# Kernel tuning notes

Hardware: AMD Instinct MI355X
Metric: run time of the kernel (lower is better)

The kernel has to match this reference:

```python
import jax, jax.numpy as jnp
import numpy as np
import math

NB = 4           # num_bands
EPS = 1e-5       # LayerNorm eps


def _dwconv(x, w):
    # depthwise Conv1d, padding=1, kernel=3. x: [b, t, c], w: [c, 1, k]
    c = x.shape[-1]
    y = jax.lax.conv_general_dilated(
        x.transpose(0, 2, 1), w, window_strides=(1,), padding=[(1, 1)],
        dimension_numbers=('NCH', 'OIH', 'NCH'), feature_group_count=c)
    return y.transpose(0, 2, 1)


def _ln(x, g, b):
    m = jnp.mean(x, axis=-1, keepdims=True)
    v = jnp.mean(jnp.square(x - m), axis=-1, keepdims=True)
    return (x - m) * jax.lax.rsqrt(v + EPS) * g + b


def _attn(x, mem, qw, qc, kw, kc, vw, vc, ow, pw, prev_qk):
    # x, mem: [b, w, c]
    b, w, c = x.shape
    d = c // NB
    q = _dwconv(x @ qw.T, qc).reshape(b, w, NB, d).transpose(0, 2, 1, 3)      # [b,nb,w,d]
    k = _dwconv(mem @ kw.T, kc).reshape(b, w, NB, d).transpose(0, 2, 3, 1)    # [b,nb,d,w]
    v = _dwconv(mem @ vw.T, vc).reshape(b, w, NB, d).transpose(0, 2, 1, 3)    # [b,nb,w,d]
    # skewed relative-position bias: matmul + pad + transpose + slice
    p = jnp.einsum('bnwd,dt->bnwt', q, pw[:, :w])                              # [b,nb,w,w]
    p = jnp.pad(p, ((0, 0), (0, 0), (0, 0), (1, 0)))                           # pad last dim left
    p = p.transpose(0, 1, 3, 2)[:, :, 1:, :]                                   # skew
    qk = (jnp.einsum('bnwd,bndt->bnwt', q, k) + p) / math.sqrt(c)
    if prev_qk is not None:
        qk = qk + prev_qk
    a = jnp.einsum('bnwt,bntd->bnwd', jax.nn.softmax(qk, axis=-1), v)
    a = a.transpose(0, 2, 1, 3).reshape(b, w, c)
    return a @ ow.T, qk


def setup_inputs() -> dict:
    key = jax.random.key(0)
    ks = jax.random.split(key, 32)
    B, CH, BINS, W, FF = 4, 8, 1024, 1024, 2048
    s = 0.02
    inp = {
        'x': jax.random.normal(ks[0], (B, CH, BINS, W), jnp.float32),
        'mem': jax.random.normal(ks[1], (B, CH, BINS, W), jnp.float32),
        'prev_qk1': jax.random.normal(ks[2], (B, NB, W, W), jnp.float32),
        'prev_qk2': jax.random.normal(ks[3], (B, NB, W, W), jnp.float32),
        'ip_w': jax.random.normal(ks[4], (CH,), jnp.float32) * s,
        'ip_b': jnp.zeros((1,), jnp.float32),
        'mp_w': jax.random.normal(ks[5], (CH,), jnp.float32) * s,
        'mp_b': jnp.zeros((1,), jnp.float32),
        'ln1_g': jnp.ones((BINS,), jnp.float32), 'ln1_b': jnp.zeros((BINS,), jnp.float32),
        'ln2_g': jnp.ones((BINS,), jnp.float32), 'ln2_b': jnp.zeros((BINS,), jnp.float32),
        'ln3_g': jnp.ones((BINS,), jnp.float32), 'ln3_b': jnp.zeros((BINS,), jnp.float32),
        'a1_qw': jax.random.normal(ks[6], (BINS, BINS), jnp.float32) * s,
        'a1_qc': jax.random.normal(ks[7], (BINS, 1, 3), jnp.float32) * 0.3,
        'a1_kw': jax.random.normal(ks[8], (BINS, BINS), jnp.float32) * s,
        'a1_kc': jax.random.normal(ks[9], (BINS, 1, 3), jnp.float32) * 0.3,
        'a1_vw': jax.random.normal(ks[10], (BINS, BINS), jnp.float32) * s,
        'a1_vc': jax.random.normal(ks[11], (BINS, 1, 3), jnp.float32) * 0.3,
        'a1_ow': jax.random.normal(ks[12], (BINS, BINS), jnp.float32) * s,
        'a1_pw': jax.random.normal(ks[13], (BINS // NB, W), jnp.float32),
        'a2_qw': jax.random.normal(ks[14], (BINS, BINS), jnp.float32) * s,
        'a2_qc': jax.random.normal(ks[15], (BINS, 1, 3), jnp.float32) * 0.3,
        'a2_kw': jax.random.normal(ks[16], (BINS, BINS), jnp.float32) * s,
        'a2_kc': jax.random.normal(ks[17], (BINS, 1, 3), jnp.float32) * 0.3,
        'a2_vw': jax.random.normal(ks[18], (BINS, BINS), jnp.float32) * s,
        'a2_vc': jax.random.normal(ks[19], (BINS, 1, 3), jnp.float32) * 0.3,
        'a2_ow': jax.random.normal(ks[20], (BINS, BINS), jnp.float32) * s,
        'a2_pw': jax.random.normal(ks[21], (BINS // NB, W), jnp.float32),
        'l1_w': jax.random.normal(ks[22], (FF, BINS), jnp.float32) * s,
        'l2_w': jax.random.normal(ks[23], (BINS, FF), jnp.float32) * s,
    }
    return inp


def reference(x, mem, prev_qk1, prev_qk2, ip_w, ip_b, mp_w, mp_b,
              ln1_g, ln1_b, ln2_g, ln2_b, ln3_g, ln3_b,
              a1_qw, a1_qc, a1_kw, a1_kc, a1_vw, a1_vc, a1_ow, a1_pw,
              a2_qw, a2_qc, a2_kw, a2_kc, a2_vw, a2_vc, a2_ow, a2_pw,
              l1_w, l2_w):
    # 1x1 Conv2d to 1 channel then [b, w, bins] layout
    xs = jnp.einsum('bchw,c->bwh', x, ip_w) + ip_b    # [b, w, bins]
    ms = jnp.einsum('bchw,c->bwh', mem, mp_w) + mp_b
    # self-attention with prev_qk residual
    h, qk1 = _attn(_ln(xs, ln1_g, ln1_b), _ln(xs, ln1_g, ln1_b),
                   a1_qw, a1_qc, a1_kw, a1_kc, a1_vw, a1_vc, a1_ow, a1_pw, prev_qk1)
    xs = xs + h
    # cross-attention against mem
    h, qk2 = _attn(_ln(xs, ln2_g, ln2_b), ms,
                   a2_qw, a2_qc, a2_kw, a2_kc, a2_vw, a2_vc, a2_ow, a2_pw, prev_qk2)
    xs = xs + h
    # squared-ReLU FFN
    h = _ln(xs, ln3_g, ln3_b)
    h = jnp.square(jax.nn.relu(h @ l1_w.T)) @ l2_w.T
    xs = xs + h
    out = xs.transpose(0, 2, 1)[:, None]              # [b, 1, bins, w]
    return (out, qk1, qk2)
```

## Files before the change

kernel.cpp:

```cpp
#include <hip/hip_runtime.h>
#include <stdint.h>

typedef unsigned short u16;
typedef __bf16 bfv8 __attribute__((ext_vector_type(8)));
typedef float f32x4 __attribute__((ext_vector_type(4)));
typedef unsigned short u16x8 __attribute__((ext_vector_type(8)));

#define DI __device__ __forceinline__

DI u16 f2bf(float f) {
  union { float f; unsigned u; } c; c.f = f;
  unsigned r = c.u + 0x7FFFu + ((c.u >> 16) & 1u);
  return (u16)(r >> 16);
}
DI float bf2f(u16 b) {
  union { unsigned u; float f; } c; c.u = ((unsigned)b) << 16;
  return c.f;
}

enum { EPI_BF16 = 0, EPI_RELU2 = 1, EPI_ADDF32 = 2, EPI_QK = 3 };

#define GLDS(g, l)                                                              \
  __builtin_amdgcn_global_load_lds((const __attribute__((address_space(1))) void*)(g), \
                                   (__attribute__((address_space(3))) void*)(l), 16, 0, 0)

#define VMCNT_BAR(N)                                        \
  do {                                                      \
    asm volatile("s_waitcnt vmcnt(" #N ")" ::: "memory");   \
    __builtin_amdgcn_sched_barrier(0);                      \
    __builtin_amdgcn_s_barrier();                           \
    __builtin_amdgcn_sched_barrier(0);                      \
  } while (0)

template <int EPI, bool KSPLIT, int BN>
__global__ __launch_bounds__(512) void gemm256(
    const u16* __restrict__ Aq, const u16* __restrict__ Akv, int asplit,
    long a1q, long a1r, int lda1,
    const u16* __restrict__ A2, int lda2,
    const u16* __restrict__ B1, long b1q, long b1r, int ldb1,
    const u16* __restrict__ B2, long b2q, long b2r, int ldb2,
    int K, int ksp,
    void* __restrict__ Cv, long cq, long cr, int ldc,
    const float* __restrict__ extra, long eq, int lde,
    float scale)
{
  constexpr int NJ = BN / 64;
  constexpr int NBL = BN / 64;
  constexpr int SS = 8192 + BN * 64;
  constexpr int LPS = 2 + NBL;
  __shared__ __align__(16) u16 lds[3 * SS];
  const int tid = threadIdx.x;
  const int wid = tid >> 6, lane = tid & 63;
  const long zq = blockIdx.z >> 2, zr = blockIdx.z & 3;
  const int m0 = blockIdx.y * 128, n0 = blockIdx.x * BN;
  const u16* Ab = ((n0 >= asplit) ? Akv : Aq) + zq * a1q + zr * a1r;
  const u16* Bb = B1 + zq * b1q + zr * b1r;
  const u16* B2b = KSPLIT ? (B2 + zq * b2q + zr * b2r) : (const u16*)nullptr;
  const int wm = (wid >> 2) * 64, wn = (wid & 3) * (BN / 4);
  const int fr = lane & 15, fq = lane >> 4;

  f32x4 acc[4][NJ];
#pragma unroll
  for (int i = 0; i < 4; ++i)
#pragma unroll
    for (int j = 0; j < NJ; ++j)
      acc[i][j] = (f32x4){0.f, 0.f, 0.f, 0.f};

  const int nt = K >> 6;

  auto STAGE = [&](int tt, int sb) {
    const int k0 = tt << 6;
    u16* Ld = &lds[sb * SS];
    const u16* Asrc; int la; const u16* Bsrc; int lb;
    if (!KSPLIT || k0 < ksp) { Asrc = Ab + k0; la = lda1; Bsrc = Bb + k0; lb = ldb1; }
    else { Asrc = A2 + (k0 - ksp); la = lda2; Bsrc = B2b + (k0 - ksp); lb = ldb2; }
#pragma unroll
    for (int l = 0; l < 2; ++l) {
      int idx = (l << 9) + tid;
      int row = idx >> 3;
      int sc = ((idx & 7) ^ (row & 7)) << 3;
      GLDS(Asrc + (size_t)(m0 + row) * la + sc,
           Ld + (((l << 3) + wid) << 9));
    }
#pragma unroll
    for (int l = 0; l < NBL; ++l) {
      int idx = (l << 9) + tid;
      int row = idx >> 3;
      int sc = ((idx & 7) ^ (row & 7)) << 3;
      GLDS(Bsrc + (size_t)(n0 + row) * lb + sc,
           Ld + 8192 + (((l << 3) + wid) << 9));
    }
  };

  auto COMPUTE = [&](int cb) {
    const u16* As = &lds[cb * SS];
    const u16* Bs = As + 8192;
#pragma unroll
    for (int ks = 0; ks < 2; ++ks) {
      bfv8 av[4];
#pragma unroll
      for (int i = 0; i < 4; ++i) {
        int ra = wm + i * 16 + fr;
        int ca = (((ks << 2) + fq) ^ (ra & 7)) << 3;
        av[i] = *(const bfv8*)&As[(ra << 6) + ca];
      }
#pragma unroll
      for (int nh = 0; nh < NJ / 2; ++nh) {
        bfv8 bv[2];
#pragma unroll
        for (int j = 0; j < 2; ++j) {
          int rb = wn + (nh << 5) + (j << 4) + fr;
          int cb2 = (((ks << 2) + fq) ^ (rb & 7)) << 3;
          bv[j] = *(const bfv8*)&Bs[(rb << 6) + cb2];
        }
        __builtin_amdgcn_s_setprio(1);
#pragma unroll
        for (int i = 0; i < 4; ++i) {
          acc[i][(nh << 1)] = __builtin_amdgcn_mfma_f32_16x16x32_bf16(av[i], bv[0], acc[i][(nh << 1)], 0, 0, 0);
          acc[i][(nh << 1) + 1] = __builtin_amdgcn_mfma_f32_16x16x32_bf16(av[i], bv[1], acc[i][(nh << 1) + 1], 0, 0, 0);
        }
        __builtin_amdgcn_s_setprio(0);
      }
    }
  };

  STAGE(0, 0);
  STAGE(1, 1);
  if constexpr (LPS == 6) VMCNT_BAR(6); else VMCNT_BAR(4);
  int cur = 0;
  for (int t = 0; t < nt; ++t) {
    if (t + 2 < nt) {
      int stg = cur + 2; if (stg >= 3) stg -= 3;
      STAGE(t + 2, stg);
      COMPUTE(cur);
      if constexpr (LPS == 6) VMCNT_BAR(6); else VMCNT_BAR(4);
    } else if (t + 1 < nt) {
      COMPUTE(cur);
      VMCNT_BAR(0);
    } else {
      COMPUTE(cur);
    }
    cur = (cur == 2) ? 0 : cur + 1;
  }

  if constexpr (EPI == EPI_BF16 || EPI == EPI_RELU2) {
    u16* Cb = (u16*)Cv + zq * cq + zr * cr;
#pragma unroll
    for (int i = 0; i < 4; ++i)
#pragma unroll
      for (int j = 0; j < NJ; ++j)
#pragma unroll
        for (int r = 0; r < 4; ++r) {
          int row = m0 + wm + i * 16 + (fq << 2) + r;
          int col = n0 + wn + j * 16 + fr;
          float v = acc[i][j][r];
          if constexpr (EPI == EPI_RELU2) { v = fmaxf(v, 0.f); v = v * v; }
          Cb[(size_t)row * ldc + col] = f2bf(v);
        }
  } else if constexpr (EPI == EPI_ADDF32) {
    float* Cb = (float*)Cv + zq * cq + zr * cr;
#pragma unroll
    for (int i = 0; i < 4; ++i)
#pragma unroll
      for (int j = 0; j < NJ; ++j)
#pragma unroll
        for (int r = 0; r < 4; ++r) {
          int row = m0 + wm + i * 16 + (fq << 2) + r;
          int col = n0 + wn + j * 16 + fr;
          Cb[(size_t)row * ldc + col] += acc[i][j][r];
        }
  } else {
    float* Cb = (float*)Cv + zq * cq + zr * cr;
    const float* Eb = extra + (size_t)blockIdx.z * eq;
#pragma unroll
    for (int i = 0; i < 4; ++i)
#pragma unroll
      for (int j = 0; j < NJ; ++j)
#pragma unroll
        for (int r = 0; r < 4; ++r) {
          int row = m0 + wm + i * 16 + (fq << 2) + r;
          int col = n0 + wn + j * 16 + fr;
          Cb[(size_t)row * ldc + col] = acc[i][j][r] * scale + Eb[(size_t)row * lde + col];
        }
  }
}

__global__ __launch_bounds__(256) void proj2v_kernel(const float* __restrict__ x,
                                                     const float* __restrict__ memp,
                                                     const float* __restrict__ ipw,
                                                     const float* __restrict__ ipb,
                                                     const float* __restrict__ mpw,
                                                     const float* __restrict__ mpb,
                                                     float* __restrict__ xs,
                                                     u16* __restrict__ msb)
{
  __shared__ float lt[64][65];
  int task = blockIdx.z >> 2;
  int b = blockIdx.z & 3;
  const float* src = task ? memp : x;
  const float* w8 = task ? mpw : ipw;
  float bias = task ? mpb[0] : ipb[0];
  int h0 = blockIdx.y * 64, w0 = blockIdx.x * 64;
  int tx = threadIdx.x & 15;
  int hy = threadIdx.x >> 4;
#pragma unroll
  for (int p = 0; p < 4; ++p) {
    int h = h0 + hy + p * 16;
    f32x4 acc = {bias, bias, bias, bias};
#pragma unroll
    for (int c = 0; c < 8; ++c) {
      f32x4 v = *(const f32x4*)&src[(((size_t)b * 8 + c) * 1024 + h) * 1024 + w0 + tx * 4];
      float wc = w8[c];
      acc.x += v.x * wc; acc.y += v.y * wc; acc.z += v.z * wc; acc.w += v.w * wc;
    }
    int hl = hy + p * 16;
    lt[tx * 4 + 0][hl] = acc.x;
    lt[tx * 4 + 1][hl] = acc.y;
    lt[tx * 4 + 2][hl] = acc.z;
    lt[tx * 4 + 3][hl] = acc.w;
  }
  __syncthreads();
  int hx = threadIdx.x & 15;
  int wy = threadIdx.x >> 4;
#pragma unroll
  for (int p = 0; p < 4; ++p) {
    int wl = wy + p * 16;
    f32x4 v;
    v.x = lt[wl][hx * 4 + 0];
    v.y = lt[wl][hx * 4 + 1];
    v.z = lt[wl][hx * 4 + 2];
    v.w = lt[wl][hx * 4 + 3];
    size_t o = ((size_t)b * 1024 + w0 + wl) * 1024 + h0 + hx * 4;
    if (task) {
      ushort4 ov;
      ov.x = f2bf(v.x); ov.y = f2bf(v.y); ov.z = f2bf(v.z); ov.w = f2bf(v.w);
      *(ushort4*)&msb[o] = ov;
    } else {
      *(f32x4*)&xs[o] = v;
    }
  }
}

__global__ __launch_bounds__(256) void ln_kernel(const float* __restrict__ x,
                                                 const float* __restrict__ g,
                                                 const float* __restrict__ b,
                                                 u16* __restrict__ out)
{
  int row = blockIdx.x, tid = threadIdx.x;
  float4 v = ((const float4*)(x + (size_t)row * 1024))[tid];
  float s = v.x + v.y + v.z + v.w;
  float s2 = v.x * v.x + v.y * v.y + v.z * v.z + v.w * v.w;
#pragma unroll
  for (int o = 32; o; o >>= 1) { s += __shfl_down(s, o); s2 += __shfl_down(s2, o); }
  __shared__ float rs[4], rs2[4];
  int wid = tid >> 6, lane = tid & 63;
  if (lane == 0) { rs[wid] = s; rs2[wid] = s2; }
  __syncthreads();
  s = rs[0] + rs[1] + rs[2] + rs[3];
  s2 = rs2[0] + rs2[1] + rs2[2] + rs2[3];
  float mean = s * (1.f / 1024.f);
  float var = s2 * (1.f / 1024.f) - mean * mean;
  float rstd = rsqrtf(var + 1e-5f);
  float4 gv = ((const float4*)g)[tid];
  float4 bv = ((const float4*)b)[tid];
  ushort4 o;
  o.x = f2bf((v.x - mean) * rstd * gv.x + bv.x);
  o.y = f2bf((v.y - mean) * rstd * gv.y + bv.y);
  o.z = f2bf((v.z - mean) * rstd * gv.z + bv.z);
  o.w = f2bf((v.w - mean) * rstd * gv.w + bv.w);
  ((ushort4*)out)[(size_t)row * 256 + tid] = o;
}

__global__ __launch_bounds__(128) void dwconv_qk_kernel(const u16* __restrict__ qkv,
                                                        const float* __restrict__ qc,
                                                        const float* __restrict__ kc,
                                                        u16* __restrict__ Qc,
                                                        u16* __restrict__ Kc)
{
  int sel = blockIdx.y;
  int row = blockIdx.x;
  int t = row & 1023;
  int c0 = threadIdx.x * 8;
  const u16* r0 = qkv + (size_t)row * 3072 + (sel << 10) + c0;
  const float* wc = sel ? kc : qc;
  u16* dst = (sel ? Kc : Qc) + (size_t)row * 1024 + c0;
  u16x8 zv = {0, 0, 0, 0, 0, 0, 0, 0};
  u16x8 xm = zv, xp = zv;
  if (t > 0) xm = *(const u16x8*)(r0 - 3072);
  u16x8 xc = *(const u16x8*)r0;
  if (t < 1023) xp = *(const u16x8*)(r0 + 3072);
  u16x8 o;
#pragma unroll
  for (int j = 0; j < 8; ++j) {
    int c = c0 + j;
    float v = bf2f(xm[j]) * wc[c * 3 + 0] + bf2f(xc[j]) * wc[c * 3 + 1] + bf2f(xp[j]) * wc[c * 3 + 2];
    o[j] = f2bf(v);
  }
  *(u16x8*)dst = o;
}

__global__ __launch_bounds__(1024) void dwconv_t_kernel(const u16* __restrict__ qkv,
                                                        const float* __restrict__ wc,
                                                        u16* __restrict__ out)
{
  __shared__ float tile[32][33];
  int b = blockIdx.z;
  int t = blockIdx.x * 32 + threadIdx.y;
  int c = blockIdx.y * 32 + threadIdx.x;
  size_t base = ((size_t)b * 1024 + t) * 3072 + 2048 + c;
  float xm = (t > 0) ? bf2f(qkv[base - 3072]) : 0.f;
  float xc = bf2f(qkv[base]);
  float xp = (t < 1023) ? bf2f(qkv[base + 3072]) : 0.f;
  tile[threadIdx.y][threadIdx.x] = xm * wc[c * 3 + 0] + xc * wc[c * 3 + 1] + xp * wc[c * 3 + 2];
  __syncthreads();
  int c2 = blockIdx.y * 32 + threadIdx.y;
  int t2 = blockIdx.x * 32 + threadIdx.x;
  int z = b * 4 + (c2 >> 8);
  out[((size_t)z * 256 + (c2 & 255)) * 1024 + t2] = f2bf(tile[threadIdx.x][threadIdx.y]);
}

__global__ __launch_bounds__(256) void softmax_kernel(const float* __restrict__ qk,
                                                      u16* __restrict__ P)
{
  size_t row = blockIdx.x;
  int tid = threadIdx.x;
  float4 v = ((const float4*)(qk + row * 1024))[tid];
  float m = fmaxf(fmaxf(v.x, v.y), fmaxf(v.z, v.w));
#pragma unroll
  for (int o = 32; o; o >>= 1) m = fmaxf(m, __shfl_down(m, o));
  __shared__ float red[4];
  int wid = tid >> 6, lane = tid & 63;
  if (lane == 0) red[wid] = m;
  __syncthreads();
  m = fmaxf(fmaxf(red[0], red[1]), fmaxf(red[2], red[3]));
  float e0 = __expf(v.x - m), e1 = __expf(v.y - m), e2 = __expf(v.z - m), e3 = __expf(v.w - m);
  float s = e0 + e1 + e2 + e3;
#pragma unroll
  for (int o = 32; o; o >>= 1) s += __shfl_down(s, o);
  __syncthreads();
  if (lane == 0) red[wid] = s;
  __syncthreads();
  s = red[0] + red[1] + red[2] + red[3];
  float rinv = 1.f / s;
  ushort4 o;
  o.x = f2bf(e0 * rinv); o.y = f2bf(e1 * rinv); o.z = f2bf(e2 * rinv); o.w = f2bf(e3 * rinv);
  ((ushort4*)P)[row * 256 + tid] = o;
}

struct CastJobs { const float* s[12]; u16* d[12]; };
__global__ __launch_bounds__(256) void cast12_kernel(CastJobs J)
{
  int j = blockIdx.y;
  int i = blockIdx.x * 256 + threadIdx.x;
  float4 v = ((const float4*)J.s[j])[i];
  ushort4 o;
  o.x = f2bf(v.x); o.y = f2bf(v.y); o.z = f2bf(v.z); o.w = f2bf(v.w);
  ((ushort4*)J.d[j])[i] = o;
}

__global__ __launch_bounds__(1024) void pwt_kernel(const float* __restrict__ pw,
                                                   u16* __restrict__ pwT)
{
  __shared__ float tile[32][33];
  int d = blockIdx.y * 32 + threadIdx.y;
  int t = blockIdx.x * 32 + threadIdx.x;
  tile[threadIdx.y][threadIdx.x] = pw[(size_t)d * 1024 + t];
  __syncthreads();
  int t2 = blockIdx.x * 32 + threadIdx.y;
  int d2 = blockIdx.y * 32 + threadIdx.x;
  pwT[(size_t)t2 * 256 + d2] = f2bf(tile[threadIdx.x][threadIdx.y]);
}

__global__ __launch_bounds__(1024) void tout_kernel(const float* __restrict__ xs,
                                                    float* __restrict__ out)
{
  __shared__ float tile[32][33];
  int b = blockIdx.z;
  int w = blockIdx.x * 32 + threadIdx.y;
  int h = blockIdx.y * 32 + threadIdx.x;
  tile[threadIdx.y][threadIdx.x] = xs[((size_t)b * 1024 + w) * 1024 + h];
  __syncthreads();
  int h2 = blockIdx.y * 32 + threadIdx.y;
  int w2 = blockIdx.x * 32 + threadIdx.x;
  out[((size_t)b * 1024 + h2) * 1024 + w2] = tile[threadIdx.x][threadIdx.y];
}

static void run_attn(hipStream_t stream, float* xs, const u16* qsrc, const u16* kvsrc, int asplit,
                     u16* QKVraw, u16* Qc, u16* Kc, u16* Vt, u16* P, u16* Am,
                     const u16* wqkv, const u16* wo, const u16* pwt,
                     const float* qc, const float* kc, const float* vc,
                     const float* prevqk, float* qko)
{
  dim3 blk(512);
  gemm256<EPI_BF16, false, 256><<<dim3(12, 32, 1), blk, 0, stream>>>(
      qsrc, kvsrc, asplit, 0, 0, 1024, nullptr, 0,
      wqkv, 0, 0, 1024, nullptr, 0, 0, 0,
      1024, 0, QKVraw, 0, 0, 3072, nullptr, 0, 0, 1.f);
  dwconv_qk_kernel<<<dim3(4096, 2), 128, 0, stream>>>(QKVraw, qc, kc, Qc, Kc);
  dwconv_t_kernel<<<dim3(32, 32, 4), dim3(32, 32), 0, stream>>>(QKVraw, vc, Vt);
  gemm256<EPI_QK, true, 256><<<dim3(4, 8, 16), blk, 0, stream>>>(
      Qc, Qc, 1 << 30, 1048576, 256, 1024, pwt, 256,
      Kc, 1048576, 256, 1024, Qc, 1048576, 256, 1024,
      512, 256, qko, 4194304, 1048576, 1024, prevqk, 1048576, 1024, 0.03125f);
  softmax_kernel<<<16384, 256, 0, stream>>>(qko, P);
  gemm256<EPI_BF16, false, 128><<<dim3(2, 8, 16), blk, 0, stream>>>(
      P, P, 1 << 30, 4194304, 1048576, 1024, nullptr, 0,
      Vt, 1048576, 262144, 1024, nullptr, 0, 0, 0,
      1024, 0, Am, 1048576, 256, 1024, nullptr, 0, 0, 1.f);
  gemm256<EPI_ADDF32, false, 128><<<dim3(8, 32, 1), blk, 0, stream>>>(
      Am, Am, 1 << 30, 0, 0, 1024, nullptr, 0,
      wo, 0, 0, 1024, nullptr, 0, 0, 0,
      1024, 0, xs, 0, 0, 1024, nullptr, 0, 0, 1.f);
}

extern "C" void kernel_launch(void* const* d_in, const int* in_sizes, int n_in,
                              void* d_out, int out_size, void* d_ws, size_t ws_size,
                              hipStream_t stream)
{
  (void)in_sizes; (void)n_in; (void)out_size; (void)ws_size;
  const float* x    = (const float*)d_in[0];
  const float* memp = (const float*)d_in[1];
  const float* pqk1 = (const float*)d_in[2];
  const float* pqk2 = (const float*)d_in[3];
  const float* ip_w = (const float*)d_in[4];
  const float* ip_b = (const float*)d_in[5];
  const float* mp_w = (const float*)d_in[6];
  const float* mp_b = (const float*)d_in[7];
  const float* ln1g = (const float*)d_in[8];
  const float* ln1b = (const float*)d_in[9];
  const float* ln2g = (const float*)d_in[10];
  const float* ln2b = (const float*)d_in[11];
  const float* ln3g = (const float*)d_in[12];
  const float* ln3b = (const float*)d_in[13];
  const float* a1qw = (const float*)d_in[14];
  const float* a1qc = (const float*)d_in[15];
  const float* a1kw = (const float*)d_in[16];
  const float* a1kc = (const float*)d_in[17];
  const float* a1vw = (const float*)d_in[18];
  const float* a1vc = (const float*)d_in[19];
  const float* a1ow = (const float*)d_in[20];
  const float* a1pw = (const float*)d_in[21];
  const float* a2qw = (const float*)d_in[22];
  const float* a2qc = (const float*)d_in[23];
  const float* a2kw = (const float*)d_in[24];
  const float* a2kc = (const float*)d_in[25];
  const float* a2vw = (const float*)d_in[26];
  const float* a2vc = (const float*)d_in[27];
  const float* a2ow = (const float*)d_in[28];
  const float* a2pw = (const float*)d_in[29];
  const float* l1w  = (const float*)d_in[30];
  const float* l2w  = (const float*)d_in[31];

  float* outp = (float*)d_out;
  float* qk1o = outp + 4194304;
  float* qk2o = outp + 20971520;

  const size_t MB = 1024 * 1024;
  char* W = (char*)d_ws;
  float* xs   = (float*)(W);
  u16* msb    = (u16*)(W + 16 * MB);
  u16* xln    = (u16*)(W + 24 * MB);
  u16* QKVraw = (u16*)(W + 32 * MB);
  u16* Qc     = (u16*)(W + 56 * MB);
  u16* Kc     = (u16*)(W + 64 * MB);
  u16* Vt     = (u16*)(W + 72 * MB);
  u16* P      = (u16*)(W + 80 * MB);
  u16* Am     = (u16*)(W + 112 * MB);
  u16* wqkv1  = (u16*)(W + 120 * MB);
  u16* wqkv2  = (u16*)(W + 126 * MB);
  u16* wo1    = (u16*)(W + 132 * MB);
  u16* wo2    = (u16*)(W + 134 * MB);
  u16* wl1    = (u16*)(W + 136 * MB);
  u16* wl2    = (u16*)(W + 140 * MB);
  u16* pwt1   = (u16*)(W + 144 * MB);
  u16* pwt2   = (u16*)(W + 144 * MB + 512 * 1024);
  u16* H1     = QKVraw;

  CastJobs J;
  J.s[0] = a1qw; J.d[0] = wqkv1;
  J.s[1] = a1kw; J.d[1] = wqkv1 + 1048576;
  J.s[2] = a1vw; J.d[2] = wqkv1 + 2097152;
  J.s[3] = a2qw; J.d[3] = wqkv2;
  J.s[4] = a2kw; J.d[4] = wqkv2 + 1048576;
  J.s[5] = a2vw; J.d[5] = wqkv2 + 2097152;
  J.s[6] = a1ow; J.d[6] = wo1;
  J.s[7] = a2ow; J.d[7] = wo2;
  J.s[8] = l1w;            J.d[8] = wl1;
  J.s[9] = l1w + 1048576;  J.d[9] = wl1 + 1048576;
  J.s[10] = l2w;           J.d[10] = wl2;
  J.s[11] = l2w + 1048576; J.d[11] = wl2 + 1048576;
  cast12_kernel<<<dim3(1024, 12), 256, 0, stream>>>(J);
  pwt_kernel<<<dim3(32, 8, 1), dim3(32, 32), 0, stream>>>(a1pw, pwt1);
  pwt_kernel<<<dim3(32, 8, 1), dim3(32, 32), 0, stream>>>(a2pw, pwt2);

  proj2v_kernel<<<dim3(16, 16, 8), 256, 0, stream>>>(
      x, memp, ip_w, ip_b, mp_w, mp_b, xs, msb);

  ln_kernel<<<4096, 256, 0, stream>>>(xs, ln1g, ln1b, xln);
  run_attn(stream, xs, xln, xln, 1 << 30, QKVraw, Qc, Kc, Vt, P, Am,
           wqkv1, wo1, pwt1, a1qc, a1kc, a1vc, pqk1, qk1o);

  ln_kernel<<<4096, 256, 0, stream>>>(xs, ln2g, ln2b, xln);
  run_attn(stream, xs, xln, msb, 1024, QKVraw, Qc, Kc, Vt, P, Am,
           wqkv2, wo2, pwt2, a2qc, a2kc, a2vc, pqk2, qk2o);

  ln_kernel<<<4096, 256, 0, stream>>>(xs, ln3g, ln3b, xln);
  gemm256<EPI_RELU2, false, 256><<<dim3(8, 32, 1), dim3(512), 0, stream>>>(
      xln, xln, 1 << 30, 0, 0, 1024, nullptr, 0,
      wl1, 0, 0, 1024, nullptr, 0, 0, 0,
      1024, 0, H1, 0, 0, 2048, nullptr, 0, 0, 1.f);
  gemm256<EPI_ADDF32, false, 128><<<dim3(8, 32, 1), dim3(512), 0, stream>>>(
      H1, H1, 1 << 30, 0, 0, 2048, nullptr, 0,
      wl2, 0, 0, 2048, nullptr, 0, 0, 0,
      2048, 0, xs, 0, 0, 1024, nullptr, 0, 0, 1.f);

  tout_kernel<<<dim3(32, 32, 4), dim3(32, 32), 0, stream>>>(xs, outp);
}
```

Measured before the change: 517.9 us.

## Remap GEMM workgroups per XCD and restructure channel-projection transpose kernel

The GEMM kernel now remaps the flat workgroup index so that consecutive logical tiles land on the same XCD. This is meant to improve L2 reuse of shared A/B tiles across the chiplets. Separately, the input projection kernel is rewritten to use 1024-thread blocks that each cover full 1024-wide rows for 16 h values. Each thread then writes 16 contiguous output elements (64B fp32 or 32B bf16), aiming for more coalesced reads and wider writes. The risks are extra index arithmetic in the GEMM and larger blocks with 64KB of LDS in the projection kernel, which can reduce occupancy.

Result: no change. 515.3 us (-0.5%).

```diff
diff --git a/kernel.cpp b/kernel.cpp
--- a/kernel.cpp
+++ b/kernel.cpp
@@ -51,8 +51,20 @@
   __shared__ __align__(16) u16 lds[3 * SS];
   const int tid = threadIdx.x;
   const int wid = tid >> 6, lane = tid & 63;
-  const long zq = blockIdx.z >> 2, zr = blockIdx.z & 3;
-  const int m0 = blockIdx.y * 128, n0 = blockIdx.x * BN;
+
+  const int gx = gridDim.x, gy = gridDim.y;
+  const int nwg = gx * gy * (int)gridDim.z;
+  const int flat = blockIdx.x + gx * (blockIdx.y + gy * blockIdx.z);
+  const int q = nwg >> 3, r = nwg & 7;
+  const int xcd = flat & 7, idx = flat >> 3;
+  const int wg = (xcd < r ? xcd * (q + 1) : r * (q + 1) + (xcd - r) * q) + idx;
+  const int bx = wg % gx;
+  const int tmp = wg / gx;
+  const int by = tmp % gy;
+  const int bz = tmp / gy;
+
+  const long zq = bz >> 2, zr = bz & 3;
+  const int m0 = by * 128, n0 = bx * BN;
   const u16* Ab = ((n0 >= asplit) ? Akv : Aq) + zq * a1q + zr * a1r;
   const u16* Bb = B1 + zq * b1q + zr * b1r;
   const u16* B2b = KSPLIT ? (B2 + zq * b2q + zr * b2r) : (const u16*)nullptr;
@@ -76,17 +88,17 @@
     else { Asrc = A2 + (k0 - ksp); la = lda2; Bsrc = B2b + (k0 - ksp); lb = ldb2; }
 #pragma unroll
     for (int l = 0; l < 2; ++l) {
-      int idx = (l << 9) + tid;
-      int row = idx >> 3;
-      int sc = ((idx & 7) ^ (row & 7)) << 3;
+      int idx2 = (l << 9) + tid;
+      int row = idx2 >> 3;
+      int sc = ((idx2 & 7) ^ (row & 7)) << 3;
       GLDS(Asrc + (size_t)(m0 + row) * la + sc,
            Ld + (((l << 3) + wid) << 9));
     }
 #pragma unroll
     for (int l = 0; l < NBL; ++l) {
-      int idx = (l << 9) + tid;
-      int row = idx >> 3;
-      int sc = ((idx & 7) ^ (row & 7)) << 3;
+      int idx2 = (l << 9) + tid;
+      int row = idx2 >> 3;
+      int sc = ((idx2 & 7) ^ (row & 7)) << 3;
       GLDS(Bsrc + (size_t)(n0 + row) * lb + sc,
            Ld + 8192 + (((l << 3) + wid) << 9));
     }
@@ -150,10 +162,10 @@
 #pragma unroll
       for (int j = 0; j < NJ; ++j)
 #pragma unroll
-        for (int r = 0; r < 4; ++r) {
-          int row = m0 + wm + i * 16 + (fq << 2) + r;
+        for (int r2 = 0; r2 < 4; ++r2) {
+          int row = m0 + wm + i * 16 + (fq << 2) + r2;
           int col = n0 + wn + j * 16 + fr;
-          float v = acc[i][j][r];
+          float v = acc[i][j][r2];
           if constexpr (EPI == EPI_RELU2) { v = fmaxf(v, 0.f); v = v * v; }
           Cb[(size_t)row * ldc + col] = f2bf(v);
         }
@@ -164,28 +176,28 @@
 #pragma unroll
       for (int j = 0; j < NJ; ++j)
 #pragma unroll
-        for (int r = 0; r < 4; ++r) {
-          int row = m0 + wm + i * 16 + (fq << 2) + r;
+        for (int r2 = 0; r2 < 4; ++r2) {
+          int row = m0 + wm + i * 16 + (fq << 2) + r2;
           int col = n0 + wn + j * 16 + fr;
-          Cb[(size_t)row * ldc + col] += acc[i][j][r];
+          Cb[(size_t)row * ldc + col] += acc[i][j][r2];
         }
   } else {
     float* Cb = (float*)Cv + zq * cq + zr * cr;
-    const float* Eb = extra + (size_t)blockIdx.z * eq;
+    const float* Eb = extra + (size_t)bz * eq;
 #pragma unroll
     for (int i = 0; i < 4; ++i)
 #pragma unroll
       for (int j = 0; j < NJ; ++j)
 #pragma unroll
-        for (int r = 0; r < 4; ++r) {
-          int row = m0 + wm + i * 16 + (fq << 2) + r;
+        for (int r2 = 0; r2 < 4; ++r2) {
+          int row = m0 + wm + i * 16 + (fq << 2) + r2;
           int col = n0 + wn + j * 16 + fr;
-          Cb[(size_t)row * ldc + col] = acc[i][j][r] * scale + Eb[(size_t)row * lde + col];
+          Cb[(size_t)row * ldc + col] = acc[i][j][r2] * scale + Eb[(size_t)row * lde + col];
         }
   }
 }
 
-__global__ __launch_bounds__(256) void proj2v_kernel(const float* __restrict__ x,
+__global__ __launch_bounds__(1024) void proj3_kernel(const float* __restrict__ x,
                                                      const float* __restrict__ memp,
                                                      const float* __restrict__ ipw,
                                                      const float* __restrict__ ipb,
@@ -194,49 +206,49 @@
                                                      float* __restrict__ xs,
                                                      u16* __restrict__ msb)
 {
-  __shared__ float lt[64][65];
-  int task = blockIdx.z >> 2;
-  int b = blockIdx.z & 3;
+  __shared__ f32x4 lt[16][256];
+  const int task = blockIdx.z;
+  const int b = blockIdx.y;
+  const int h0 = blockIdx.x * 16;
   const float* src = task ? memp : x;
   const float* w8 = task ? mpw : ipw;
-  float bias = task ? mpb[0] : ipb[0];
-  int h0 = blockIdx.y * 64, w0 = blockIdx.x * 64;
-  int tx = threadIdx.x & 15;
-  int hy = threadIdx.x >> 4;
+  const float bias = task ? mpb[0] : ipb[0];
+  const int t = threadIdx.x;
+  const int w4 = t & 255, hl = t >> 8;
+  float wr[8];
+#pragma unroll
+  for (int c = 0; c < 8; ++c) wr[c] = w8[c];
 #pragma unroll
   for (int p = 0; p < 4; ++p) {
-    int h = h0 + hy + p * 16;
+    const int hr = p * 4 + hl;
+    const size_t rowbase = ((size_t)b * 8 * 1024 + (h0 + hr)) * 1024 + (w4 << 2);
     f32x4 acc = {bias, bias, bias, bias};
 #pragma unroll
     for (int c = 0; c < 8; ++c) {
-      f32x4 v = *(const f32x4*)&src[(((size_t)b * 8 + c) * 1024 + h) * 1024 + w0 + tx * 4];
-      float wc = w8[c];
-      acc.x += v.x * wc; acc.y += v.y * wc; acc.z += v.z * wc; acc.w += v.w * wc;
+      f32x4 v = *(const f32x4*)&src[rowbase + (size_t)c * 1048576];
+      acc.x += v.x * wr[c]; acc.y += v.y * wr[c]; acc.z += v.z * wr[c]; acc.w += v.w * wr[c];
     }
-    int hl = hy + p * 16;
-    lt[tx * 4 + 0][hl] = acc.x;
-    lt[tx * 4 + 1][hl] = acc.y;
-    lt[tx * 4 + 2][hl] = acc.z;
-    lt[tx * 4 + 3][hl] = acc.w;
+    lt[hr][w4] = acc;
   }
   __syncthreads();
-  int hx = threadIdx.x & 15;
-  int wy = threadIdx.x >> 4;
-#pragma unroll
-  for (int p = 0; p < 4; ++p) {
-    int wl = wy + p * 16;
-    f32x4 v;
-    v.x = lt[wl][hx * 4 + 0];
-    v.y = lt[wl][hx * 4 + 1];
-    v.z = lt[wl][hx * 4 + 2];
-    v.w = lt[wl][hx * 4 + 3];
-    size_t o = ((size_t)b * 1024 + w0 + wl) * 1024 + h0 + hx * 4;
-    if (task) {
-      ushort4 ov;
-      ov.x = f2bf(v.x); ov.y = f2bf(v.y); ov.z = f2bf(v.z); ov.w = f2bf(v.w);
-      *(ushort4*)&msb[o] = ov;
-    } else {
-      *(f32x4*)&xs[o] = v;
+  const int w = t;
+  float o[16];
+#pragma unroll
+  for (int h = 0; h < 16; ++h)
+    o[h] = ((const float*)&lt[h][0])[w];
+  if (task) {
+    u16* d = &msb[((size_t)b * 1024 + w) * 1024 + h0];
+    u16x8 o0, o1;
+#pragma unroll
+    for (int h = 0; h < 8; ++h) { o0[h] = f2bf(o[h]); o1[h] = f2bf(o[h + 8]); }
+    *(u16x8*)&d[0] = o0;
+    *(u16x8*)&d[8] = o1;
+  } else {
+    float* d = &xs[((size_t)b * 1024 + w) * 1024 + h0];
+#pragma unroll
+    for (int p = 0; p < 4; ++p) {
+      f32x4 v = {o[p * 4], o[p * 4 + 1], o[p * 4 + 2], o[p * 4 + 3]};
+      *(f32x4*)&d[p * 4] = v;
     }
   }
 }
@@ -493,7 +505,7 @@
   pwt_kernel<<<dim3(32, 8, 1), dim3(32, 32), 0, stream>>>(a1pw, pwt1);
   pwt_kernel<<<dim3(32, 8, 1), dim3(32, 32), 0, stream>>>(a2pw, pwt2);
 
-  proj2v_kernel<<<dim3(16, 16, 8), 256, 0, stream>>>(
+  proj3_kernel<<<dim3(64, 4, 2), 1024, 0, stream>>>(
       x, memp, ip_w, ip_b, mp_w, mp_b, xs, msb);
 
   ln_kernel<<<4096, 256, 0, stream>>>(xs, ln1g, ln1b, xln);
```
